# Optimization experiments

Hardware: AMD Instinct MI355X
Metric: run time of the kernel (lower is better)

Reference implementation:

```python
import jax, jax.numpy as jnp
import numpy as np
import math

B, L, D, H = 2, 2048, 1024, 16
DH = D // H
TAU = 1.0
EPS_LN = 1e-12


def neural_sort(scores, tau=TAU):
    # scores: (B, n) -> soft permutation P_hat: (B, n, n)
    s = scores[..., None]                                   # (B,n,1)
    A = jnp.abs(s - jnp.swapaxes(s, 1, 2))                  # (B,n,n) pairwise |s_i - s_j|
    Bsum = jnp.sum(A, axis=-1, keepdims=True)               # row sums == A @ ones(n,n) columns
    n = scores.shape[-1]
    scaling = (n + 1 - 2 * (jnp.arange(n) + 1)).astype(scores.dtype)  # (n,)
    C = s * scaling[None, None, :]                          # (B,n,n)
    P_max = jnp.swapaxes(C - Bsum, 1, 2)
    return jax.nn.softmax(P_max / tau, axis=-1)


def euler_transform(v, delta, b_euler, log_scale, is_query):
    # v: (B,L,D); soft-sort channels, polar decompose, rotate, recompose
    Bv, Lv, Dv = v.shape
    scores = v.mean(axis=1)                                 # (B,D)
    P = neural_sort(scores)                                 # (B,D,D)
    v_sorted = jnp.einsum('bij,blj->bli', P, v)             # permute channel dim
    r, p = v_sorted[..., ::2], v_sorted[..., 1::2]          # (B,L,D/2)
    lam = jnp.sqrt(r * r + p * p + 1e-6)
    lam_d = jax.lax.stop_gradient(lam)
    theta = jnp.arctan2(p / lam_d, r / lam_d)
    theta = theta * delta
    if is_query:
        theta = theta + b_euler
    lam = lam * jnp.exp(jnp.clip(log_scale, -5.0, 5.0))
    out = jnp.stack([lam * jnp.cos(theta), lam * jnp.sin(theta)], axis=-1)
    return out.reshape(Bv, Lv, Dv)


def layer_norm(x, gamma, beta, eps=EPS_LN):
    mu = x.mean(axis=-1, keepdims=True)
    var = ((x - mu) ** 2).mean(axis=-1, keepdims=True)
    return (x - mu) / jnp.sqrt(var + eps) * gamma + beta


def forward(input_tensor, Wq, bq, Wk, bk, Wv, bv, Wd, bd, gamma, beta, delta, b_euler, log_scale):
    q = input_tensor @ Wq.T + bq
    k = input_tensor @ Wk.T + bk
    v = input_tensor @ Wv.T + bv
    q = euler_transform(q, delta, b_euler, log_scale, is_query=True)
    k = euler_transform(k, delta, b_euler, log_scale, is_query=False)
    def heads(x):
        return x.reshape(B, L, H, DH).transpose(0, 2, 1, 3)  # (B,H,L,DH)
    qh, kh, vh = heads(q), heads(k), heads(v)
    scores = jnp.einsum('bhqd,bhkd->bhqk', qh, kh) / math.sqrt(DH)
    probs = jax.nn.softmax(scores, axis=-1)                 # dropout off (eval)
    ctx = jnp.einsum('bhqk,bhkd->bhqd', probs, vh)
    ctx = ctx.transpose(0, 2, 1, 3).reshape(B, L, D)
    hidden = ctx @ Wd.T + bd
    return layer_norm(hidden + input_tensor, gamma, beta)


def setup_inputs() -> dict:
    key = jax.random.key(0)
    ks = jax.random.split(key, 16)
    s = 1.0 / math.sqrt(D)
    return {
        'input_tensor': jax.random.normal(ks[0], (B, L, D), jnp.float32),
        'Wq': jax.random.normal(ks[1], (D, D), jnp.float32) * s,
        'bq': jnp.zeros((D,), jnp.float32),
        'Wk': jax.random.normal(ks[2], (D, D), jnp.float32) * s,
        'bk': jnp.zeros((D,), jnp.float32),
        'Wv': jax.random.normal(ks[3], (D, D), jnp.float32) * s,
        'bv': jnp.zeros((D,), jnp.float32),
        'Wd': jax.random.normal(ks[4], (D, D), jnp.float32) * s,
        'bd': jnp.zeros((D,), jnp.float32),
        'gamma': jnp.ones((D,), jnp.float32),
        'beta': jnp.zeros((D,), jnp.float32),
        'delta': jnp.full((1, 1, D // 2), 0.1, jnp.float32),
        'b_euler': jnp.zeros((1, 1, D // 2), jnp.float32),
        'log_scale': jnp.zeros((1, 1, D // 2), jnp.float32),
    }


def reference(input_tensor, Wq, bq, Wk, bk, Wv, bv, Wd, bd, gamma, beta, delta, b_euler, log_scale):
    return forward(input_tensor, Wq, bq, Wk, bk, Wv, bv, Wd, bd, gamma, beta, delta, b_euler, log_scale)
```

## Files before the change

### kernel.cpp

```cpp
#include <hip/hip_runtime.h>


typedef unsigned short bf16_t;
typedef short frag_ab __attribute__((ext_vector_type(8)));
typedef float frag_cd __attribute__((ext_vector_type(4)));
typedef float f32x16 __attribute__((ext_vector_type(16)));

#define BB 2
#define LL 2048
#define DD 1024
#define HH 16
#define DH 64

#define QSCALE 0.18033688f
#define EOFF  -17.3123404907f

__device__ __forceinline__ float b2f(bf16_t u) {
  union { unsigned int i; float f; } c; c.i = ((unsigned int)u) << 16; return c.f;
}
__device__ __forceinline__ bf16_t f2b(float f) {
  union { float f; unsigned int i; } c; c.f = f;
  unsigned int r = c.i + 0x7fffu + ((c.i >> 16) & 1u);
  return (bf16_t)(r >> 16);
}
__device__ __forceinline__ unsigned int fbits(float f) {
  union { float f; unsigned int i; } c; c.f = f; return c.i;
}
__device__ __forceinline__ float waveMax(float v) {
#pragma unroll
  for (int m = 32; m > 0; m >>= 1) v = fmaxf(v, __shfl_xor(v, m));
  return v;
}
__device__ __forceinline__ float waveSum(float v) {
#pragma unroll
  for (int m = 32; m > 0; m >>= 1) v += __shfl_xor(v, m);
  return v;
}

__device__ __forceinline__ void gll16(const bf16_t* g, bf16_t* l) {
  __builtin_amdgcn_global_load_lds(
      (const __attribute__((address_space(1))) void*)g,
      (__attribute__((address_space(3))) void*)l, 16, 0, 0);
}

__device__ __forceinline__ frag_ab ld_tile(const bf16_t* base, int row, int chunk) {
  return *(const frag_ab*)((const char*)base + (row << 7) + (((chunk ^ row) & 7) << 4));
}

__device__ __forceinline__ frag_ab pack8(const float* p) {
  union { unsigned int u[4]; frag_ab f; } x;
  x.u[0] = __builtin_amdgcn_perm(fbits(p[1]), fbits(p[0]), 0x07060302u);
  x.u[1] = __builtin_amdgcn_perm(fbits(p[3]), fbits(p[2]), 0x07060302u);
  x.u[2] = __builtin_amdgcn_perm(fbits(p[5]), fbits(p[4]), 0x07060302u);
  x.u[3] = __builtin_amdgcn_perm(fbits(p[7]), fbits(p[6]), 0x07060302u);
  return x.f;
}

__global__ __launch_bounds__(256) void prep_cast(const float* __restrict__ X,
                                                 const float* __restrict__ Wv,
                                                 const float* __restrict__ Wd,
                                                 bf16_t* __restrict__ Xb,
                                                 bf16_t* __restrict__ Wvb,
                                                 bf16_t* __restrict__ Wdb,
                                                 float* __restrict__ xmean) {
  const int bid = blockIdx.x;
  if (bid == 6144) {
    if (threadIdx.x < 256)
      for (int i = threadIdx.x; i < BB * DD; i += 256) xmean[i] = 0.f;
    return;
  }
  const float* in;
  bf16_t* out;
  int i;
  if (bid < 4096)      { in = X;  out = Xb;  i = bid * 256 + threadIdx.x; }
  else if (bid < 5120) { in = Wv; out = Wvb; i = (bid - 4096) * 256 + threadIdx.x; }
  else                 { in = Wd; out = Wdb; i = (bid - 5120) * 256 + threadIdx.x; }
  float4 v = ((const float4*)in)[i];
  ushort4 o;
  o.x = f2b(v.x); o.y = f2b(v.y); o.z = f2b(v.z); o.w = f2b(v.w);
  ((ushort4*)out)[i] = o;
}

__global__ __launch_bounds__(256) void cast_transpose_w(const float* __restrict__ Wq,
                                                        const float* __restrict__ Wk,
                                                        bf16_t* __restrict__ WqT,
                                                        bf16_t* __restrict__ WkT) {
  const float* W = blockIdx.z ? Wk : Wq;
  bf16_t* WT = blockIdx.z ? WkT : WqT;
  __shared__ bf16_t T[64][72];
  const int i0 = blockIdx.x * 64, m0 = blockIdx.y * 64;
  const int tid = threadIdx.x;
#pragma unroll
  for (int it = 0; it < 4; ++it) {
    const int idx = tid + it * 256;
    const int r = idx >> 4, c4 = (idx & 15) * 4;
    float4 v = *(const float4*)&W[(size_t)(i0 + r) * DD + m0 + c4];
    T[c4 + 0][r] = f2b(v.x);
    T[c4 + 1][r] = f2b(v.y);
    T[c4 + 2][r] = f2b(v.z);
    T[c4 + 3][r] = f2b(v.w);
  }
  __syncthreads();
#pragma unroll
  for (int it = 0; it < 2; ++it) {
    const int idx = tid + it * 256;
    const int r = idx >> 3, seg = idx & 7;
    *(uint4*)&WT[(size_t)(m0 + r) * DD + i0 + seg * 8] = *(const uint4*)&T[r][seg * 8];
  }
}

struct GemmB { const bf16_t* A; const bf16_t* Bm; const float* bias; float* Cf; bf16_t* Cb; };
struct GemmArgs { GemmB gb[6]; };

__global__ __launch_bounds__(256) void gemm128(GemmArgs ga, int M, int N, int K) {
  const GemmB g = ga.gb[blockIdx.z];
  const int bm = blockIdx.y * 128, bn = blockIdx.x * 128;
  __shared__ bf16_t As[128][32];
  __shared__ bf16_t Bs[128][32];
  bf16_t* As_f = &As[0][0];
  bf16_t* Bs_f = &Bs[0][0];
  const int tid = threadIdx.x;
  const int lane = tid & 63, w = tid >> 6;
  const int quad = lane >> 4, l16 = lane & 15;
  const int wm = (w >> 1) * 64, wn = (w & 1) * 64;
  const int wbase = w << 9;

  frag_cd acc[4][4];
#pragma unroll
  for (int i = 0; i < 4; ++i)
#pragma unroll
    for (int j = 0; j < 4; ++j)
#pragma unroll
      for (int r = 0; r < 4; ++r) acc[i][j][r] = 0.f;

  const int r0 = tid >> 2, s0 = (tid & 3) * 8;
  const int r1 = (tid + 256) >> 2, s1 = ((tid + 256) & 3) * 8;
  const size_t aoff0 = (size_t)(bm + r0) * K + s0;
  const size_t aoff1 = (size_t)(bm + r1) * K + s1;
  const size_t boff0 = (size_t)(bn + r0) * K + s0;
  const size_t boff1 = (size_t)(bn + r1) * K + s1;

  for (int k0 = 0; k0 < K; k0 += 32) {
    __syncthreads();
    gll16(g.A + aoff0 + k0, As_f + wbase);
    gll16(g.A + aoff1 + k0, As_f + 2048 + wbase);
    gll16(g.Bm + boff0 + k0, Bs_f + wbase);
    gll16(g.Bm + boff1 + k0, Bs_f + 2048 + wbase);
    __syncthreads();
    frag_ab af[4], bfr[4];
#pragma unroll
    for (int i = 0; i < 4; ++i) {
      af[i]  = *(const frag_ab*)&As[wm + i * 16 + l16][quad * 8];
      bfr[i] = *(const frag_ab*)&Bs[wn + i * 16 + l16][quad * 8];
    }
#pragma unroll
    for (int i = 0; i < 4; ++i)
#pragma unroll
      for (int j = 0; j < 4; ++j)
        acc[i][j] = __builtin_amdgcn_mfma_f32_16x16x32_bf16(af[i], bfr[j], acc[i][j], 0, 0, 0);
  }

#pragma unroll
  for (int i = 0; i < 4; ++i) {
#pragma unroll
    for (int r = 0; r < 4; ++r) {
      const int row = bm + wm + i * 16 + quad * 4 + r;
#pragma unroll
      for (int j = 0; j < 4; ++j) {
        const int col = bn + wn + j * 16 + l16;
        float v = acc[i][j][r];
        if (g.bias) v += g.bias[col];
        if (g.Cf) g.Cf[(size_t)row * N + col] = v;
        if (g.Cb) g.Cb[(size_t)row * N + col] = f2b(v);
      }
    }
  }
}

__global__ __launch_bounds__(256) void gemm64x64(GemmArgs ga, int M, int N, int K) {
  const GemmB g = ga.gb[blockIdx.z];
  const int bm = blockIdx.y * 64, bn = blockIdx.x * 64;
  __shared__ bf16_t As[64][32];
  __shared__ bf16_t Bs[64][32];
  bf16_t* As_f = &As[0][0];
  bf16_t* Bs_f = &Bs[0][0];
  const int tid = threadIdx.x;
  const int lane = tid & 63, w = tid >> 6;
  const int quad = lane >> 4, l16 = lane & 15;
  const int wm = (w >> 1) * 32, wn = (w & 1) * 32;
  const int wbase = w << 9;

  frag_cd acc[2][2];
#pragma unroll
  for (int i = 0; i < 2; ++i)
#pragma unroll
    for (int j = 0; j < 2; ++j)
#pragma unroll
      for (int r = 0; r < 4; ++r) acc[i][j][r] = 0.f;

  const int r0 = tid >> 2, s0 = (tid & 3) * 8;
  const size_t aoff0 = (size_t)(bm + r0) * K + s0;
  const size_t boff0 = (size_t)(bn + r0) * K + s0;

  for (int k0 = 0; k0 < K; k0 += 32) {
    __syncthreads();
    gll16(g.A + aoff0 + k0, As_f + wbase);
    gll16(g.Bm + boff0 + k0, Bs_f + wbase);
    __syncthreads();
    frag_ab af[2], bfr[2];
#pragma unroll
    for (int i = 0; i < 2; ++i) {
      af[i]  = *(const frag_ab*)&As[wm + i * 16 + l16][quad * 8];
      bfr[i] = *(const frag_ab*)&Bs[wn + i * 16 + l16][quad * 8];
    }
#pragma unroll
    for (int i = 0; i < 2; ++i)
#pragma unroll
      for (int j = 0; j < 2; ++j)
        acc[i][j] = __builtin_amdgcn_mfma_f32_16x16x32_bf16(af[i], bfr[j], acc[i][j], 0, 0, 0);
  }

#pragma unroll
  for (int i = 0; i < 2; ++i) {
#pragma unroll
    for (int r = 0; r < 4; ++r) {
      const int row = bm + wm + i * 16 + quad * 4 + r;
#pragma unroll
      for (int j = 0; j < 2; ++j) {
        const int col = bn + wn + j * 16 + l16;
        float v = acc[i][j][r];
        if (g.bias) v += g.bias[col];
        if (g.Cf) g.Cf[(size_t)row * N + col] = v;
        if (g.Cb) g.Cb[(size_t)row * N + col] = f2b(v);
      }
    }
  }
}

__global__ __launch_bounds__(256) void xmean_kernel(const float* __restrict__ X,
                                                    float* __restrict__ xmean) {
  const int d = blockIdx.x * 256 + threadIdx.x;
  const int b = blockIdx.z;
  const int l0 = blockIdx.y * 64;
  float s = 0.f;
  for (int l = l0; l < l0 + 64; ++l)
    s += X[((size_t)b * LL + l) * DD + d];
  atomicAdd(&xmean[b * DD + d], s * (1.f / (float)LL));
}

__global__ __launch_bounds__(256) void scores_gemm(const float* __restrict__ xmean,
                                                   const float* __restrict__ Wq,
                                                   const float* __restrict__ bq,
                                                   const float* __restrict__ Wk,
                                                   const float* __restrict__ bk,
                                                   float* __restrict__ scores) {
  const int w = threadIdx.x >> 6, lane = threadIdx.x & 63;
  const int idx = blockIdx.x * 4 + w;
  const int t = idx >> 11, b = (idx >> 10) & 1, i = idx & 1023;
  const float* W = t ? Wk : Wq;
  const float* bias = t ? bk : bq;
  const float* xm = xmean + b * DD;
  float sum = 0.f;
#pragma unroll
  for (int k = 0; k < 4; ++k) {
    float4 wv = *(const float4*)&W[(size_t)i * DD + k * 256 + lane * 4];
    float4 xv = *(const float4*)&xm[k * 256 + lane * 4];
    sum += wv.x * xv.x + wv.y * xv.y + wv.z * xv.z + wv.w * xv.w;
  }
  sum = waveSum(sum);
  if (lane == 0) scores[idx] = sum + bias[i];
}

__global__ __launch_bounds__(256) void bsum_kernel(const float* __restrict__ scores,
                                                   float* __restrict__ bsum) {
  __shared__ float sc[DD];
  const int z = blockIdx.x, jb = blockIdx.y, tid = threadIdx.x;
#pragma unroll
  for (int s = 0; s < 4; ++s) sc[tid + s * 256] = scores[z * DD + tid + s * 256];
  __syncthreads();
  const int j = jb * 256 + tid;
  const float si = sc[j];
  float s = 0.f;
  for (int m = 0; m < DD; m += 4) {
    float4 v = *(const float4*)&sc[m];
    s += fabsf(si - v.x) + fabsf(si - v.y) + fabsf(si - v.z) + fabsf(si - v.w);
  }
  bsum[z * DD + j] = s;
}

__global__ __launch_bounds__(256) void p_kernel(const float* __restrict__ scores,
                                                const float* __restrict__ bsum,
                                                const float* __restrict__ bq,
                                                const float* __restrict__ bk,
                                                bf16_t* __restrict__ Pq,
                                                bf16_t* __restrict__ Pk,
                                                float* __restrict__ bias4) {
  const int i = blockIdx.x;
  const int z = blockIdx.y;
  const int t = z >> 1, b = z & 1;
  const float* sc = scores + z * DD;
  const float* bs = bsum + z * DD;
  const float* bias = t ? bk : bq;
  const float scal = 1023.f - 2.f * (float)i;
  const int tid = threadIdx.x;
  __shared__ float redA[4], redB[4], redC[4];

  float lg[4], bb[4];
  float mx = -1e30f;
#pragma unroll
  for (int s = 0; s < 4; ++s) {
    const int j = tid + s * 256;
    lg[s] = sc[j] * scal - bs[j];
    bb[s] = bias[j];
    mx = fmaxf(mx, lg[s]);
  }
  mx = waveMax(mx);
  if ((tid & 63) == 0) redA[tid >> 6] = mx;
  __syncthreads();
  const float M = fmaxf(fmaxf(redA[0], redA[1]), fmaxf(redA[2], redA[3]));
  float sum = 0.f, dot = 0.f;
#pragma unroll
  for (int s = 0; s < 4; ++s) {
    lg[s] = __expf(lg[s] - M);
    sum += lg[s];
    dot += lg[s] * bb[s];
  }
  sum = waveSum(sum); dot = waveSum(dot);
  if ((tid & 63) == 0) { redB[tid >> 6] = sum; redC[tid >> 6] = dot; }
  __syncthreads();
  const float inv = 1.f / (redB[0] + redB[1] + redB[2] + redB[3]);
  bf16_t* P = (t ? Pk : Pq) + ((size_t)b << 20) + (size_t)i * DD;
#pragma unroll
  for (int s = 0; s < 4; ++s) P[tid + s * 256] = f2b(lg[s] * inv);
  if (tid == 0)
    bias4[t * 2048 + b * 1024 + i] = (redC[0] + redC[1] + redC[2] + redC[3]) * inv;
}

__global__ __launch_bounds__(256) void euler_transv(bf16_t* __restrict__ qs,
                                                    bf16_t* __restrict__ ks,
                                                    const float* __restrict__ delta,
                                                    const float* __restrict__ beul,
                                                    const float* __restrict__ lsc,
                                                    const bf16_t* __restrict__ vb,
                                                    bf16_t* __restrict__ vbT) {
  __shared__ bf16_t T[64][72];
  const int bid = blockIdx.x;
  const int tid = threadIdx.x;
  if (bid < 16384) {
    const int isq = (bid < 8192);
    unsigned int* buf = (unsigned int*)(isq ? qs : ks);
    const int idx = (isq ? bid : bid - 8192) * 256 + tid;
    const int c = idx & 511;
    const size_t n = idx >> 9;
    const unsigned int u = buf[n * 512 + c];
    const float r = b2f((bf16_t)(u & 0xffffu));
    const float p = b2f((bf16_t)(u >> 16));
    float lam = sqrtf(r * r + p * p + 1e-6f);
    float th = atan2f(p, r) * delta[c];
    if (isq) th += beul[c];
    lam *= __expf(fminf(fmaxf(lsc[c], -5.f), 5.f));
    if (isq) lam *= QSCALE;
    float sn, cs;
    __sincosf(th, &sn, &cs);
    buf[n * 512 + c] = ((unsigned int)f2b(lam * sn) << 16) | (unsigned int)f2b(lam * cs);
    return;
  }
  const int tb = bid - 16384;
  const int l0 = (tb & 31) * 64, d0 = ((tb >> 5) & 15) * 64, b = tb >> 9;
  for (int i = tid; i < 512; i += 256) {
    const int r = i >> 3, seg = i & 7;
    uint4 v = *(const uint4*)&vb[((size_t)b * LL + l0 + r) * DD + d0 + seg * 8];
    const bf16_t* vs = (const bf16_t*)&v;
#pragma unroll
    for (int j = 0; j < 8; ++j) T[seg * 8 + j][r] = vs[j];
  }
  __syncthreads();
  for (int i = tid; i < 512; i += 256) {
    const int r = i >> 3, seg = i & 7;
    const int kb = (seg >> 1) * 16 + (seg & 1) * 4;
    uint2 lo = *(const uint2*)&T[r][kb];
    uint2 hi2 = *(const uint2*)&T[r][kb + 8];
    uint4 o; o.x = lo.x; o.y = lo.y; o.z = hi2.x; o.w = hi2.y;
    *(uint4*)&vbT[((size_t)b * DD + d0 + r) * LL + l0 + seg * 8] = o;
  }
}

__global__ __launch_bounds__(256) void attn_kernel(const bf16_t* __restrict__ Q,
                                                   const bf16_t* __restrict__ Kt,
                                                   const bf16_t* __restrict__ VT,
                                                   bf16_t* __restrict__ O) {
  const int bid = blockIdx.x;
  const int swz = (bid & 7) * 64 + (bid >> 3);
  const int g = swz >> 4;
  const int qt = swz & 15;
  const int b = g >> 4, h = g & 15;
  const int q0 = qt * 128;
  const int tid = threadIdx.x, w = tid >> 6, lane = tid & 63;
  const int hi = lane >> 5, l31 = lane & 31;

  __shared__ bf16_t Ks[2][64 * 64];
  __shared__ bf16_t Vs[2][64 * 64];

  const size_t base = (size_t)b * LL * DD + (size_t)h * DH;
  const size_t vtb = (size_t)(b * DD + h * DH) * LL;

  frag_ab bq[4];
#pragma unroll
  for (int kd = 0; kd < 4; ++kd)
    bq[kd] = *(const frag_ab*)
        &Q[base + (size_t)(q0 + w * 32 + l31) * DD + kd * 16 + hi * 8];

  frag_ab bone;
  {
    const short o = (l31 == 0) ? (short)0x3F80 : (short)0;
#pragma unroll
    for (int j = 0; j < 8; ++j) bone[j] = o;
  }

  f32x16 o_[2], l5;
#pragma unroll
  for (int i = 0; i < 16; ++i) { o_[0][i] = 0.f; o_[1][i] = 0.f; l5[i] = 0.f; }

  const int srow = lane >> 3;
  const int cg = (lane & 7) ^ srow;
  const int rbase = w * 16;

  auto STAGE = [&](int buf, int kt) {
#pragma unroll
    for (int t = 0; t < 2; ++t) {
      const int row = rbase + t * 8 + srow;
      gll16(Kt + base + (size_t)(kt * 64 + row) * DD + cg * 8,
            &Ks[buf][(rbase + t * 8) * 64]);
      gll16(VT + vtb + (size_t)row * LL + kt * 64 + cg * 8,
            &Vs[buf][(rbase + t * 8) * 64]);
    }
  };

  STAGE(0, 0);
  int cur = 0;
  const int NT = LL / 64;
  for (int kt = 0; kt < NT; ++kt) {
    if (kt + 1 < NT) {
      STAGE(cur ^ 1, kt + 1);
      asm volatile("s_waitcnt vmcnt(4)" ::: "memory");
    } else {
      asm volatile("s_waitcnt vmcnt(0)" ::: "memory");
    }
    __builtin_amdgcn_s_barrier();

    const bf16_t* Kb = Ks[cur];
    const bf16_t* Vb = Vs[cur];

    frag_ab pa[4];
#pragma unroll
    for (int s = 0; s < 2; ++s) {
      frag_ab ak[4];
#pragma unroll
      for (int kd = 0; kd < 4; ++kd)
        ak[kd] = ld_tile(Kb, s * 32 + l31, kd * 2 + hi);
      f32x16 z;
#pragma unroll
      for (int i = 0; i < 16; ++i) z[i] = EOFF;
#pragma unroll
      for (int kd = 0; kd < 4; ++kd)
        z = __builtin_amdgcn_mfma_f32_32x32x16_bf16(ak[kd], bq[kd], z, 0, 0, 0);
#pragma unroll
      for (int t = 0; t < 2; ++t) {
        float p[8];
#pragma unroll
        for (int j = 0; j < 8; ++j) p[j] = __builtin_amdgcn_exp2f(z[t * 8 + j]);
        pa[s * 2 + t] = pack8(p);
      }
    }

#pragma unroll
    for (int k = 0; k < 4; ++k)
      l5 = __builtin_amdgcn_mfma_f32_32x32x16_bf16(pa[k], bone, l5, 0, 0, 0);

#pragma unroll
    for (int dt = 0; dt < 2; ++dt)
#pragma unroll
      for (int k = 0; k < 4; ++k) {
        frag_ab bv = ld_tile(Vb, dt * 32 + l31, k * 2 + hi);
        o_[dt] = __builtin_amdgcn_mfma_f32_32x32x16_bf16(pa[k], bv, o_[dt], 0, 0, 0);
      }

    __builtin_amdgcn_s_barrier();
    cur ^= 1;
  }

  const int src = (lane >> 5) << 5;
  float lf[16];
#pragma unroll
  for (int r = 0; r < 16; ++r) lf[r] = 1.f / __shfl(l5[r], src);

#pragma unroll
  for (int dt = 0; dt < 2; ++dt)
#pragma unroll
    for (int r = 0; r < 16; ++r) {
      const int ql = (r & 3) + 8 * (r >> 2) + 4 * hi;
      O[base + (size_t)(q0 + w * 32 + ql) * DD + dt * 32 + l31] =
          f2b(o_[dt][r] * lf[r]);
    }
}

__global__ __launch_bounds__(256) void ln_kernel(const bf16_t* __restrict__ hidden,
                                                 const float* __restrict__ x0,
                                                 const float* __restrict__ gamma,
                                                 const float* __restrict__ beta,
                                                 float* __restrict__ out) {
  const int row = blockIdx.x;
  const int tid = threadIdx.x;
  __shared__ float red1[4], red2[4];
  float v[4];
  float s1 = 0.f, s2 = 0.f;
#pragma unroll
  for (int s = 0; s < 4; ++s) {
    const int c = tid + s * 256;
    const float x = b2f(hidden[(size_t)row * DD + c]) + x0[(size_t)row * DD + c];
    v[s] = x; s1 += x; s2 += x * x;
  }
  s1 = waveSum(s1); s2 = waveSum(s2);
  if ((tid & 63) == 0) { red1[tid >> 6] = s1; red2[tid >> 6] = s2; }
  __syncthreads();
  const float t1 = red1[0] + red1[1] + red1[2] + red1[3];
  const float t2 = red2[0] + red2[1] + red2[2] + red2[3];
  const float mu = t1 * (1.f / DD);
  const float var = t2 * (1.f / DD) - mu * mu;
  const float inv = rsqrtf(var + 1e-12f);
#pragma unroll
  for (int s = 0; s < 4; ++s) {
    const int c = tid + s * 256;
    out[(size_t)row * DD + c] = (v[s] - mu) * inv * gamma[c] + beta[c];
  }
}

extern "C" void kernel_launch(void* const* d_in, const int* in_sizes, int n_in,
                              void* d_out, int out_size, void* d_ws, size_t ws_size,
                              hipStream_t stream) {
  const float* X    = (const float*)d_in[0];
  const float* Wq   = (const float*)d_in[1];
  const float* bq   = (const float*)d_in[2];
  const float* Wk   = (const float*)d_in[3];
  const float* bk   = (const float*)d_in[4];
  const float* Wv   = (const float*)d_in[5];
  const float* bv   = (const float*)d_in[6];
  const float* Wd   = (const float*)d_in[7];
  const float* bd   = (const float*)d_in[8];
  const float* gam  = (const float*)d_in[9];
  const float* bet  = (const float*)d_in[10];
  const float* delt = (const float*)d_in[11];
  const float* beul = (const float*)d_in[12];
  const float* lsc  = (const float*)d_in[13];
  float* out = (float*)d_out;

  char* w = (char*)d_ws;
  const size_t MB = 1024ull * 1024ull;
  bf16_t* Xb  = (bf16_t*)(w + 0 * MB);
  bf16_t* Wvb = (bf16_t*)(w + 8 * MB);
  bf16_t* Wdb = (bf16_t*)(w + 10 * MB);
  bf16_t* WqT = (bf16_t*)(w + 12 * MB);
  bf16_t* WkT = (bf16_t*)(w + 14 * MB);
  bf16_t* Pq  = (bf16_t*)(w + 16 * MB);
  bf16_t* Pk  = (bf16_t*)(w + 20 * MB);
  bf16_t* Wp  = (bf16_t*)(w + 24 * MB);
  bf16_t* vb  = (bf16_t*)(w + 32 * MB);
  bf16_t* qs  = (bf16_t*)(w + 40 * MB);
  bf16_t* ks  = (bf16_t*)(w + 48 * MB);
  bf16_t* vbT = (bf16_t*)(w + 56 * MB);
  bf16_t* ctx = (bf16_t*)(w + 64 * MB);
  bf16_t* hid = (bf16_t*)(w + 24 * MB);
  float*  xmean  = (float*)(w + 72 * MB);
  float*  scores = (float*)(w + 72 * MB + 16384);
  float*  bsum   = (float*)(w + 72 * MB + 32768);
  float*  bias4  = (float*)(w + 72 * MB + 49152);

  const size_t WSZ = (size_t)DD * DD;

  prep_cast<<<dim3(6145), 256, 0, stream>>>(X, Wv, Wd, Xb, Wvb, Wdb, xmean);
  cast_transpose_w<<<dim3(16, 16, 2), 256, 0, stream>>>(Wq, Wk, WqT, WkT);

  xmean_kernel<<<dim3(4, 32, 2), 256, 0, stream>>>(X, xmean);
  scores_gemm<<<dim3(1024), 256, 0, stream>>>(xmean, Wq, bq, Wk, bk, scores);

  bsum_kernel<<<dim3(4, 4), 256, 0, stream>>>(scores, bsum);
  p_kernel<<<dim3(1024, 4), 256, 0, stream>>>(scores, bsum, bq, bk, Pq, Pk, bias4);

  GemmArgs gw = {};
  gw.gb[0] = {Pq,       WqT, nullptr, nullptr, Wp};
  gw.gb[1] = {Pq + WSZ, WqT, nullptr, nullptr, Wp + WSZ};
  gw.gb[2] = {Pk,       WkT, nullptr, nullptr, Wp + 2 * WSZ};
  gw.gb[3] = {Pk + WSZ, WkT, nullptr, nullptr, Wp + 3 * WSZ};
  gemm64x64<<<dim3(16, 16, 4), 256, 0, stream>>>(gw, DD, DD, DD);

  const size_t XHALF = (size_t)LL * DD;
  GemmArgs gs = {};
  gs.gb[0] = {Xb,         Wp,           bias4,        nullptr, qs};
  gs.gb[1] = {Xb + XHALF, Wp + WSZ,     bias4 + 1024, nullptr, qs + XHALF};
  gs.gb[2] = {Xb,         Wp + 2 * WSZ, bias4 + 2048, nullptr, ks};
  gs.gb[3] = {Xb + XHALF, Wp + 3 * WSZ, bias4 + 3072, nullptr, ks + XHALF};
  gs.gb[4] = {Xb,         Wvb,          bv,           nullptr, vb};
  gs.gb[5] = {Xb + XHALF, Wvb,          bv,           nullptr, vb + XHALF};
  gemm128<<<dim3(8, 16, 6), 256, 0, stream>>>(gs, LL, DD, DD);

  euler_transv<<<dim3(17408), 256, 0, stream>>>(qs, ks, delt, beul, lsc, vb, vbT);

  attn_kernel<<<dim3(512), 256, 0, stream>>>(qs, ks, vbT, ctx);

  GemmArgs g4 = {};
  g4.gb[0] = {ctx, Wdb, bd, nullptr, hid};
  gemm64x64<<<dim3(16, 64, 1), 256, 0, stream>>>(g4, BB * LL, DD, DD);

  ln_kernel<<<dim3(BB * LL), 256, 0, stream>>>(hid, X, gam, bet, out);
}
```

Baseline: 291.4 us.

## Double-buffer LDS tiles in GEMM kernels to overlap global loads with MFMA

Both the 128x128 and 64x64 GEMM kernels now keep two LDS buffers per operand. The next K-slice is issued with direct global-to-LDS loads before the current slice is computed, and partial vmcnt waits plus raw s_barrier replace the two __syncthreads per iteration. The aim is to hide global memory latency behind the MFMA work. In exchange the kernels use twice the LDS, which can lower occupancy. The hand-written waitcnt/barrier sequence also relies on the compiler not reordering the LDS reads, which is a correctness risk.

```diff
diff --git a/kernel.cpp b/kernel.cpp
--- a/kernel.cpp
+++ b/kernel.cpp
@@ -115,10 +115,8 @@
 __global__ __launch_bounds__(256) void gemm128(GemmArgs ga, int M, int N, int K) {
   const GemmB g = ga.gb[blockIdx.z];
   const int bm = blockIdx.y * 128, bn = blockIdx.x * 128;
-  __shared__ bf16_t As[128][32];
-  __shared__ bf16_t Bs[128][32];
-  bf16_t* As_f = &As[0][0];
-  bf16_t* Bs_f = &Bs[0][0];
+  __shared__ bf16_t As[2][128][32];
+  __shared__ bf16_t Bs[2][128][32];
   const int tid = threadIdx.x;
   const int lane = tid & 63, w = tid >> 6;
   const int quad = lane >> 4, l16 = lane & 15;
@@ -140,24 +138,38 @@
   const size_t boff0 = (size_t)(bn + r0) * K + s0;
   const size_t boff1 = (size_t)(bn + r1) * K + s1;
 
+  auto STAGE = [&](int buf, int k0) {
+    bf16_t* Af = &As[buf][0][0];
+    bf16_t* Bf = &Bs[buf][0][0];
+    gll16(g.A + aoff0 + k0, Af + wbase);
+    gll16(g.A + aoff1 + k0, Af + 2048 + wbase);
+    gll16(g.Bm + boff0 + k0, Bf + wbase);
+    gll16(g.Bm + boff1 + k0, Bf + 2048 + wbase);
+  };
+
+  STAGE(0, 0);
+  int cur = 0;
   for (int k0 = 0; k0 < K; k0 += 32) {
-    __syncthreads();
-    gll16(g.A + aoff0 + k0, As_f + wbase);
-    gll16(g.A + aoff1 + k0, As_f + 2048 + wbase);
-    gll16(g.Bm + boff0 + k0, Bs_f + wbase);
-    gll16(g.Bm + boff1 + k0, Bs_f + 2048 + wbase);
-    __syncthreads();
+    if (k0 + 32 < K) {
+      STAGE(cur ^ 1, k0 + 32);
+      asm volatile("s_waitcnt vmcnt(4)" ::: "memory");
+    } else {
+      asm volatile("s_waitcnt vmcnt(0)" ::: "memory");
+    }
+    __builtin_amdgcn_s_barrier();
     frag_ab af[4], bfr[4];
 #pragma unroll
     for (int i = 0; i < 4; ++i) {
-      af[i]  = *(const frag_ab*)&As[wm + i * 16 + l16][quad * 8];
-      bfr[i] = *(const frag_ab*)&Bs[wn + i * 16 + l16][quad * 8];
+      af[i]  = *(const frag_ab*)&As[cur][wm + i * 16 + l16][quad * 8];
+      bfr[i] = *(const frag_ab*)&Bs[cur][wn + i * 16 + l16][quad * 8];
     }
 #pragma unroll
     for (int i = 0; i < 4; ++i)
 #pragma unroll
       for (int j = 0; j < 4; ++j)
         acc[i][j] = __builtin_amdgcn_mfma_f32_16x16x32_bf16(af[i], bfr[j], acc[i][j], 0, 0, 0);
+    __builtin_amdgcn_s_barrier();
+    cur ^= 1;
   }
 
 #pragma unroll
@@ -180,10 +192,8 @@
 __global__ __launch_bounds__(256) void gemm64x64(GemmArgs ga, int M, int N, int K) {
   const GemmB g = ga.gb[blockIdx.z];
   const int bm = blockIdx.y * 64, bn = blockIdx.x * 64;
-  __shared__ bf16_t As[64][32];
-  __shared__ bf16_t Bs[64][32];
-  bf16_t* As_f = &As[0][0];
-  bf16_t* Bs_f = &Bs[0][0];
+  __shared__ bf16_t As[2][64][32];
+  __shared__ bf16_t Bs[2][64][32];
   const int tid = threadIdx.x;
   const int lane = tid & 63, w = tid >> 6;
   const int quad = lane >> 4, l16 = lane & 15;
@@ -202,22 +212,34 @@
   const size_t aoff0 = (size_t)(bm + r0) * K + s0;
   const size_t boff0 = (size_t)(bn + r0) * K + s0;
 
+  auto STAGE = [&](int buf, int k0) {
+    gll16(g.A + aoff0 + k0, &As[buf][0][0] + wbase);
+    gll16(g.Bm + boff0 + k0, &Bs[buf][0][0] + wbase);
+  };
+
+  STAGE(0, 0);
+  int cur = 0;
   for (int k0 = 0; k0 < K; k0 += 32) {
-    __syncthreads();
-    gll16(g.A + aoff0 + k0, As_f + wbase);
-    gll16(g.Bm + boff0 + k0, Bs_f + wbase);
-    __syncthreads();
+    if (k0 + 32 < K) {
+      STAGE(cur ^ 1, k0 + 32);
+      asm volatile("s_waitcnt vmcnt(2)" ::: "memory");
+    } else {
+      asm volatile("s_waitcnt vmcnt(0)" ::: "memory");
+    }
+    __builtin_amdgcn_s_barrier();
     frag_ab af[2], bfr[2];
 #pragma unroll
     for (int i = 0; i < 2; ++i) {
-      af[i]  = *(const frag_ab*)&As[wm + i * 16 + l16][quad * 8];
-      bfr[i] = *(const frag_ab*)&Bs[wn + i * 16 + l16][quad * 8];
+      af[i]  = *(const frag_ab*)&As[cur][wm + i * 16 + l16][quad * 8];
+      bfr[i] = *(const frag_ab*)&Bs[cur][wn + i * 16 + l16][quad * 8];
     }
 #pragma unroll
     for (int i = 0; i < 2; ++i)
 #pragma unroll
       for (int j = 0; j < 2; ++j)
         acc[i][j] = __builtin_amdgcn_mfma_f32_16x16x32_bf16(af[i], bfr[j], acc[i][j], 0, 0, 0);
+    __builtin_amdgcn_s_barrier();
+    cur ^= 1;
   }
 
 #pragma unroll
```

Measured after the change: 277.7 us. -4.7%, faster.
